# Optimization experiments

Hardware: AMD Instinct MI355X
Metric: run time of the kernel (lower is better)

Reference implementation:

```python
import jax, jax.numpy as jnp
import numpy as np

NUM_HEADS = 16
HEAD_DIM = 64  # hidden_size 1024 / 16 heads


def setup_inputs() -> dict:
    key = jax.random.key(0)
    ks = jax.random.split(key, 9)
    B, T, H = 8, 4096, 1024
    s = 1.0 / np.sqrt(H)
    return {
        "hidden_states": jax.random.normal(ks[0], (B, T + 1, H), jnp.float32),
        "cell_state": jax.random.normal(ks[1], (B, H), jnp.float32),
        "Wq": jax.random.normal(ks[2], (H, H), jnp.float32) * s,
        "bq": jax.random.normal(ks[3], (H,), jnp.float32) * 0.02,
        "Wk": jax.random.normal(ks[4], (H, H), jnp.float32) * s,
        "bk": jax.random.normal(ks[5], (H,), jnp.float32) * 0.02,
        "Wv": jax.random.normal(ks[6], (H, H), jnp.float32) * s,
        "bv": jax.random.normal(ks[7], (H,), jnp.float32) * 0.02,
        "attention_mask": jax.random.randint(ks[8], (B, T), 0, 2, jnp.int32),
        "t": T,
    }


def reference(hidden_states, cell_state, Wq, bq, Wk, bk, Wv, bv, attention_mask, t):
    B, _, H = hidden_states.shape
    nh, hd = NUM_HEADS, HEAD_DIM
    # single-query projection: [B, H] -> [B, nh, hd]
    q = (cell_state @ Wq.T + bq).reshape(B, nh, hd)
    # key/value over first t positions: [B, t, H] -> [B, t, nh, hd]
    kv_in = hidden_states[:, :-1]
    k = (kv_in @ Wk.T + bk).reshape(B, t, nh, hd)
    v = (kv_in @ Wv.T + bv).reshape(B, t, nh, hd)
    # GEMV-like scores: [B, nh, t]
    scores = jnp.einsum("bhd,bthd->bht", q, k) / np.sqrt(hd)
    # mask out positions where attention_mask == 0 (intended semantics of
    # inf * eq(mask, 0) in the original, expressed without -inf*0 NaNs)
    mask_add = jnp.where(attention_mask == 0, -jnp.inf, 0.0)[:, None, :]
    probs = jax.nn.softmax(scores + mask_add, axis=-1)
    # dropout is identity in eval mode
    ctx = jnp.einsum("bht,bthd->bhd", probs, v)  # [B, nh, hd]
    return ctx.reshape(B, nh * hd)  # squeeze of [B, 1, H]
```

## Files before the change

kernel.cpp:

```cpp
#include <hip/hip_runtime.h>
#include <math.h>

#define BB 8
#define TT 4096
#define TP1 4097
#define HH 1024
#define NHD 16

__device__ __forceinline__ float dot4(const float4& a, const float4& b) {
  return a.x*b.x + a.y*b.y + a.z*b.z + a.w*b.w;
}

__global__ __launch_bounds__(256) void k_q(const float* __restrict__ cell,
                                           const float* __restrict__ Wq,
                                           const float* __restrict__ bq,
                                           float* __restrict__ qbuf) {
  __shared__ float cs[BB * HH];
  int tid = threadIdx.x;
  #pragma unroll
  for (int m = 0; m < 8; m++) {
    int idx4 = tid + (m << 8);
    ((float4*)cs)[idx4] = ((const float4*)cell)[idx4];
  }
  __syncthreads();
  int jj = tid >> 6, lane = tid & 63;
  int j = blockIdx.x * 4 + jj;
  float acc[BB];
  #pragma unroll
  for (int b = 0; b < BB; b++) acc[b] = 0.f;
  #pragma unroll
  for (int k = 0; k < 4; k++) {
    int i = (k << 8) + (lane << 2);
    float4 w = *(const float4*)&Wq[(size_t)j * HH + i];
    #pragma unroll
    for (int b = 0; b < BB; b++) acc[b] += dot4(w, *(const float4*)&cs[b * HH + i]);
  }
  #pragma unroll
  for (int b = 0; b < BB; b++) {
    acc[b] += __shfl_xor(acc[b], 1);  acc[b] += __shfl_xor(acc[b], 2);
    acc[b] += __shfl_xor(acc[b], 4);  acc[b] += __shfl_xor(acc[b], 8);
    acc[b] += __shfl_xor(acc[b], 16); acc[b] += __shfl_xor(acc[b], 32);
  }
  if (lane == 0) {
    float bqv = bq[j];
    #pragma unroll
    for (int b = 0; b < BB; b++) qbuf[b * HH + j] = 0.125f * (acc[b] + bqv);
  }
}

__global__ __launch_bounds__(256) void k_qwk(const float* __restrict__ qbuf,
                                             const float* __restrict__ Wk,
                                             const float* __restrict__ bk,
                                             float* __restrict__ qWkT,
                                             float* __restrict__ qbk) {
  __shared__ float q_s[BB * 64];
  __shared__ float red[4 * 64 * 9];
  int tid = threadIdx.x;
  int h = blockIdx.x >> 4, ic = blockIdx.x & 15;
  if (tid < 128) {
    int b = tid >> 4, dq = tid & 15;
    ((float4*)q_s)[tid] = ((const float4*)qbuf)[(b << 8) + (h << 4) + dq];
  }
  __syncthreads();
  int dg = tid >> 6, lane = tid & 63;
  int i = (ic << 6) + lane;
  float acc[BB];
  #pragma unroll
  for (int b = 0; b < BB; b++) acc[b] = 0.f;
  #pragma unroll
  for (int dd = 0; dd < 16; dd++) {
    int d = (dg << 4) + dd;
    float wk = Wk[(size_t)((h << 6) + d) * HH + i];
    #pragma unroll
    for (int b = 0; b < BB; b++) acc[b] += q_s[(b << 6) + d] * wk;
  }
  #pragma unroll
  for (int b = 0; b < BB; b++) red[((dg << 6) + lane) * 9 + b] = acc[b];
  __syncthreads();
  #pragma unroll
  for (int r = 0; r < 2; r++) {
    int o = tid + (r << 8);
    int il = o >> 3, b = o & 7;
    float s = 0.f;
    #pragma unroll
    for (int g = 0; g < 4; g++) s += red[((g << 6) + il) * 9 + b];
    qWkT[((size_t)(b << 10) + (ic << 6) + il) * NHD + h] = s;
  }
  if (ic == 0 && tid < 8) {
    float s = 0.f;
    for (int d = 0; d < 64; d++) s += q_s[(tid << 6) + d] * bk[(h << 6) + d];
    qbk[tid * NHD + h] = s;
  }
}

__global__ __launch_bounds__(512) void k_sctx(const float* __restrict__ hid,
                                              const float* __restrict__ qWkT,
                                              const float* __restrict__ qbk,
                                              const int* __restrict__ mask,
                                              float* __restrict__ ctxp,
                                              float* __restrict__ Spart) {
  __shared__ float S[16384];
  __shared__ float E[1280];
  int tid = threadIdx.x;
  int b = blockIdx.x >> 6, g = blockIdx.x & 63;
  int t0 = g << 6;
  int w = __builtin_amdgcn_readfirstlane(tid >> 6);
  int lane = tid & 63;
  const float* src = hid + ((size_t)b * TP1 + t0) * HH;
  int sub = lane >> 5, q31 = lane & 31;

  #define STAGE(cc, buf)                                                            \
    {                                                                               \
      _Pragma("unroll")                                                             \
      for (int j = 0; j < 4; j++) {                                                 \
        int row0 = (w << 3) + (j << 1);                                             \
        int row = row0 + sub;                                                       \
        const float* gp = src + (size_t)row * HH + ((cc) << 7) +                    \
                          ((q31 ^ (row & 7)) << 2);                                 \
        float* dp = &S[((buf) << 13) + row0 * 128];                                 \
        __builtin_amdgcn_global_load_lds(                                           \
            (const __attribute__((address_space(1))) unsigned int*)gp,              \
            (__attribute__((address_space(3))) unsigned int*)dp, 16, 0, 0);         \
      }                                                                             \
    }

  STAGE(0, 0);
  __syncthreads();

  float acc[16];
  #pragma unroll
  for (int h = 0; h < 16; h++) acc[h] = 0.f;
  const float* qb = qWkT + ((size_t)b << 14);

  for (int c = 0; c < 8; c++) {
    if (c < 7) STAGE(c + 1, (c + 1) & 1);
    const float* sb = &S[(c & 1) << 13];
    #pragma unroll
    for (int s = 0; s < 4; s++) {
      int q = (w << 2) + s;
      float4 kvq = *(const float4*)&sb[lane * 128 + ((q ^ (lane & 7)) << 2)];
      const float* qp = qb + (((size_t)(c << 7) + (q << 2)) << 4);
      #pragma unroll
      for (int ii = 0; ii < 4; ii++) {
        float kvv = (ii == 0) ? kvq.x : (ii == 1) ? kvq.y : (ii == 2) ? kvq.z : kvq.w;
        const float* qi = qp + (ii << 4);
        float4 q0 = *(const float4*)(qi);
        float4 q1 = *(const float4*)(qi + 4);
        float4 q2 = *(const float4*)(qi + 8);
        float4 q3 = *(const float4*)(qi + 12);
        acc[0]  += kvv * q0.x;  acc[1]  += kvv * q0.y;
        acc[2]  += kvv * q0.z;  acc[3]  += kvv * q0.w;
        acc[4]  += kvv * q1.x;  acc[5]  += kvv * q1.y;
        acc[6]  += kvv * q1.z;  acc[7]  += kvv * q1.w;
        acc[8]  += kvv * q2.x;  acc[9]  += kvv * q2.y;
        acc[10] += kvv * q2.z;  acc[11] += kvv * q2.w;
        acc[12] += kvv * q3.x;  acc[13] += kvv * q3.y;
        acc[14] += kvv * q3.z;  acc[15] += kvv * q3.w;
      }
    }
    __syncthreads();
  }

  {
    float* rp = S + w * 1088 + lane * 17;
    #pragma unroll
    for (int h = 0; h < 16; h++) rp[h] = acc[h];
  }
  __syncthreads();

  {
    float s1 = 0.f, s2 = 0.f;
    #pragma unroll
    for (int ww = 0; ww < 8; ww++) {
      s1 += S[ww * 1088 + lane * 17 + w];
      s2 += S[ww * 1088 + lane * 17 + w + 8];
    }
    s1 += qbk[b * NHD + w];
    s2 += qbk[b * NHD + w + 8];
    int mk = mask[b * TT + t0 + lane];
    float e1 = mk ? __expf(s1) : 0.f;
    float e2 = mk ? __expf(s2) : 0.f;
    E[lane * 20 + w] = e1;
    E[lane * 20 + w + 8] = e2;
    float sp1 = e1, sp2 = e2;
    #pragma unroll
    for (int m2 = 1; m2 < 64; m2 <<= 1) {
      sp1 += __shfl_xor(sp1, m2);
      sp2 += __shfl_xor(sp2, m2);
    }
    if (lane == 0) {
      Spart[(((size_t)b << 6) + g) * NHD + w] = sp1;
      Spart[(((size_t)b << 6) + g) * NHD + w + 8] = sp2;
    }
  }
  __syncthreads();

  STAGE(0, 0);
  __syncthreads();

  for (int c = 0; c < 8; c++) {
    if (c < 7) STAGE(c + 1, (c + 1) & 1);
    if (w < 4) {
      float4 p0 = make_float4(0.f, 0.f, 0.f, 0.f);
      float4 p1 = make_float4(0.f, 0.f, 0.f, 0.f);
      float4 p2 = make_float4(0.f, 0.f, 0.f, 0.f);
      float4 p3 = make_float4(0.f, 0.f, 0.f, 0.f);
      const float* sb = &S[(c & 1) << 13];
      #pragma unroll 8
      for (int r = 0; r < 32; r++) {
        int row = (sub << 5) + r;
        float4 kvq = *(const float4*)&sb[row * 128 + ((q31 ^ (row & 7)) << 2)];
        float4 ev  = *(const float4*)&E[row * 20 + (w << 2)];
        p0.x += kvq.x * ev.x; p0.y += kvq.y * ev.x; p0.z += kvq.z * ev.x; p0.w += kvq.w * ev.x;
        p1.x += kvq.x * ev.y; p1.y += kvq.y * ev.y; p1.z += kvq.z * ev.y; p1.w += kvq.w * ev.y;
        p2.x += kvq.x * ev.z; p2.y += kvq.y * ev.z; p2.z += kvq.z * ev.z; p2.w += kvq.w * ev.z;
        p3.x += kvq.x * ev.w; p3.y += kvq.y * ev.w; p3.z += kvq.z * ev.w; p3.w += kvq.w * ev.w;
      }
      p0.x += __shfl_xor(p0.x, 32); p0.y += __shfl_xor(p0.y, 32);
      p0.z += __shfl_xor(p0.z, 32); p0.w += __shfl_xor(p0.w, 32);
      p1.x += __shfl_xor(p1.x, 32); p1.y += __shfl_xor(p1.y, 32);
      p1.z += __shfl_xor(p1.z, 32); p1.w += __shfl_xor(p1.w, 32);
      p2.x += __shfl_xor(p2.x, 32); p2.y += __shfl_xor(p2.y, 32);
      p2.z += __shfl_xor(p2.z, 32); p2.w += __shfl_xor(p2.w, 32);
      p3.x += __shfl_xor(p3.x, 32); p3.y += __shfl_xor(p3.y, 32);
      p3.z += __shfl_xor(p3.z, 32); p3.w += __shfl_xor(p3.w, 32);
      if (sub == 0) {
        float* cp = ctxp + ((((size_t)(b << 6) + g) * NHD + (w << 2)) << 10) +
                    (c << 7) + (q31 << 2);
        *(float4*)(cp)        = p0;
        *(float4*)(cp + 1024) = p1;
        *(float4*)(cp + 2048) = p2;
        *(float4*)(cp + 3072) = p3;
      }
    }
    __syncthreads();
  }
  #undef STAGE
}

__global__ void k_sinv(const float* __restrict__ Spart, float* __restrict__ Sinv) {
  int tid = threadIdx.x;
  int b = tid >> 4, h = tid & 15;
  float s = 0.f;
  #pragma unroll 8
  for (int c = 0; c < 64; c++) s += Spart[(size_t)((b << 6) + c) * NHD + h];
  Sinv[tid] = 1.f / s;
}

__global__ __launch_bounds__(256) void k_reduce(const float* __restrict__ ctxp,
                                                float* __restrict__ ctxin) {
  int tid = threadIdx.x;
  int b = blockIdx.x >> 4, h = blockIdx.x & 15;
  const float4* cp4 = (const float4*)ctxp;
  float4 s = make_float4(0.f, 0.f, 0.f, 0.f);
  #pragma unroll 8
  for (int g = 0; g < 64; g++) {
    float4 v = cp4[((((size_t)b * 64 + g) * 16 + h) << 8) + tid];
    s.x += v.x; s.y += v.y; s.z += v.z; s.w += v.w;
  }
  ((float4*)ctxin)[(((size_t)(b << 4) + h) << 8) + tid] = s;
}

__global__ __launch_bounds__(256) void k_out(const float* __restrict__ Wv,
                                             const float* __restrict__ bv,
                                             const float* __restrict__ ctxin,
                                             const float* __restrict__ Sinv,
                                             float* __restrict__ out) {
  __shared__ float cs[BB * HH];
  int tid = threadIdx.x;
  int h = blockIdx.x >> 4;
  int j0 = blockIdx.x * 4;
  #pragma unroll
  for (int m = 0; m < 8; m++) {
    int idx4 = tid + (m << 8);
    int b = idx4 >> 8, i4 = idx4 & 255;
    ((float4*)cs)[idx4] = ((const float4*)ctxin)[(((b << 4) + h) << 8) + i4];
  }
  __syncthreads();
  int jj = tid >> 6, lane = tid & 63;
  int j = j0 + jj;
  float acc[BB];
  #pragma unroll
  for (int b = 0; b < BB; b++) acc[b] = 0.f;
  #pragma unroll
  for (int k = 0; k < 4; k++) {
    int i = (k << 8) + (lane << 2);
    float4 w = *(const float4*)&Wv[(size_t)j * HH + i];
    #pragma unroll
    for (int b = 0; b < BB; b++) acc[b] += dot4(w, *(const float4*)&cs[b * HH + i]);
  }
  #pragma unroll
  for (int b = 0; b < BB; b++) {
    acc[b] += __shfl_xor(acc[b], 1);  acc[b] += __shfl_xor(acc[b], 2);
    acc[b] += __shfl_xor(acc[b], 4);  acc[b] += __shfl_xor(acc[b], 8);
    acc[b] += __shfl_xor(acc[b], 16); acc[b] += __shfl_xor(acc[b], 32);
  }
  if (lane == 0) {
    float bvj = bv[j];
    #pragma unroll
    for (int b = 0; b < BB; b++)
      out[b * HH + j] = Sinv[b * NHD + h] * acc[b] + bvj;
  }
}

extern "C" void kernel_launch(void* const* d_in, const int* in_sizes, int n_in,
                              void* d_out, int out_size, void* d_ws, size_t ws_size,
                              hipStream_t stream) {
  const float* hid  = (const float*)d_in[0];
  const float* cell = (const float*)d_in[1];
  const float* Wq   = (const float*)d_in[2];
  const float* bq   = (const float*)d_in[3];
  const float* Wk   = (const float*)d_in[4];
  const float* bk   = (const float*)d_in[5];
  const float* Wv   = (const float*)d_in[6];
  const float* bv   = (const float*)d_in[7];
  const int*  mask  = (const int*)d_in[8];
  float* out = (float*)d_out;

  float* ws = (float*)d_ws;
  float* qbuf    = ws;
  float* qWkT    = ws + 8192;
  float* qbk     = ws + 139264;
  float* Spart   = ws + 139392;
  float* Sinv    = ws + 147584;
  float* ctxin   = ws + 147712;
  float* ctxp    = ws + 278784;

  hipLaunchKernelGGL(k_q,      dim3(256), dim3(256), 0, stream, cell, Wq, bq, qbuf);
  hipLaunchKernelGGL(k_qwk,    dim3(256), dim3(256), 0, stream, qbuf, Wk, bk, qWkT, qbk);
  hipLaunchKernelGGL(k_sctx,   dim3(512), dim3(512), 0, stream, hid, qWkT, qbk, mask, ctxp, Spart);
  hipLaunchKernelGGL(k_sinv,   dim3(1),   dim3(128), 0, stream, Spart, Sinv);
  hipLaunchKernelGGL(k_reduce, dim3(128), dim3(256), 0, stream, ctxp, ctxin);
  hipLaunchKernelGGL(k_out,    dim3(256), dim3(256), 0, stream, Wv, bv, ctxin, Sinv, out);
}
```

Baseline: 266.0 us.

## Halve k_sctx LDS staging chunks and fold softmax-sum kernel into k_out

The score/context kernel now stages 64-column chunks instead of 128 (16 chunks instead of 8) and reuses the staging buffer for the exp values, cutting shared memory from about 69KB to about 37KB so more blocks can be resident per CU. The cross-wave score reduction is reworked to fit the smaller buffer, and the PV loop uses 16-lane groups with an extra shuffle stage. The single-block k_sinv launch is removed; k_out sums the partial softmax denominators itself. In exchange there are twice as many barriers and stage loops, and every k_out block repeats the denominator reduction.

```diff
diff --git a/kernel.cpp b/kernel.cpp
--- a/kernel.cpp
+++ b/kernel.cpp
@@ -99,25 +99,25 @@
                                               const int* __restrict__ mask,
                                               float* __restrict__ ctxp,
                                               float* __restrict__ Spart) {
-  __shared__ float S[16384];
-  __shared__ float E[1280];
+  __shared__ float S[9472];
   int tid = threadIdx.x;
   int b = blockIdx.x >> 6, g = blockIdx.x & 63;
   int t0 = g << 6;
   int w = __builtin_amdgcn_readfirstlane(tid >> 6);
   int lane = tid & 63;
   const float* src = hid + ((size_t)b * TP1 + t0) * HH;
-  int sub = lane >> 5, q31 = lane & 31;
+  int rsub = lane >> 4, q15 = lane & 15;
+  #define E_OFF 8192
 
   #define STAGE(cc, buf)                                                            \
     {                                                                               \
       _Pragma("unroll")                                                             \
-      for (int j = 0; j < 4; j++) {                                                 \
-        int row0 = (w << 3) + (j << 1);                                             \
-        int row = row0 + sub;                                                       \
-        const float* gp = src + (size_t)row * HH + ((cc) << 7) +                    \
-                          ((q31 ^ (row & 7)) << 2);                                 \
-        float* dp = &S[((buf) << 13) + row0 * 128];                                 \
+      for (int j = 0; j < 2; j++) {                                                 \
+        int row0 = (w << 3) + (j << 2);                                             \
+        int row = row0 + rsub;                                                      \
+        const float* gp = src + (size_t)row * HH + ((cc) << 6) +                    \
+                          ((q15 ^ (row & 7)) << 2);                                 \
+        float* dp = &S[((buf) << 12) + (row0 << 6)];                                \
         __builtin_amdgcn_global_load_lds(                                           \
             (const __attribute__((address_space(1))) unsigned int*)gp,              \
             (__attribute__((address_space(3))) unsigned int*)dp, 16, 0, 0);         \
@@ -132,14 +132,14 @@
   for (int h = 0; h < 16; h++) acc[h] = 0.f;
   const float* qb = qWkT + ((size_t)b << 14);
 
-  for (int c = 0; c < 8; c++) {
-    if (c < 7) STAGE(c + 1, (c + 1) & 1);
-    const float* sb = &S[(c & 1) << 13];
-    #pragma unroll
-    for (int s = 0; s < 4; s++) {
-      int q = (w << 2) + s;
-      float4 kvq = *(const float4*)&sb[lane * 128 + ((q ^ (lane & 7)) << 2)];
-      const float* qp = qb + (((size_t)(c << 7) + (q << 2)) << 4);
+  for (int c = 0; c < 16; c++) {
+    if (c < 15) STAGE(c + 1, (c + 1) & 1);
+    const float* sb = &S[(c & 1) << 12];
+    #pragma unroll
+    for (int s = 0; s < 2; s++) {
+      int q = (w << 1) + s;
+      float4 kvq = *(const float4*)&sb[(lane << 6) + ((q ^ (lane & 7)) << 2)];
+      const float* qp = qb + (((size_t)(c << 6) + (q << 2)) << 4);
       #pragma unroll
       for (int ii = 0; ii < 4; ii++) {
         float kvv = (ii == 0) ? kvq.x : (ii == 1) ? kvq.y : (ii == 2) ? kvq.z : kvq.w;
@@ -161,27 +161,33 @@
     __syncthreads();
   }
 
-  {
+  if (w >= 4) {
+    float* rp = S + (w - 4) * 1088 + lane * 17;
+    #pragma unroll
+    for (int h = 0; h < 16; h++) rp[h] = acc[h];
+  }
+  __syncthreads();
+  if (w < 4) {
     float* rp = S + w * 1088 + lane * 17;
     #pragma unroll
-    for (int h = 0; h < 16; h++) rp[h] = acc[h];
+    for (int h = 0; h < 16; h++) rp[h] += acc[h];
   }
   __syncthreads();
 
   {
     float s1 = 0.f, s2 = 0.f;
     #pragma unroll
-    for (int ww = 0; ww < 8; ww++) {
-      s1 += S[ww * 1088 + lane * 17 + w];
-      s2 += S[ww * 1088 + lane * 17 + w + 8];
+    for (int ss = 0; ss < 4; ss++) {
+      s1 += S[ss * 1088 + lane * 17 + w];
+      s2 += S[ss * 1088 + lane * 17 + w + 8];
     }
     s1 += qbk[b * NHD + w];
     s2 += qbk[b * NHD + w + 8];
     int mk = mask[b * TT + t0 + lane];
     float e1 = mk ? __expf(s1) : 0.f;
     float e2 = mk ? __expf(s2) : 0.f;
-    E[lane * 20 + w] = e1;
-    E[lane * 20 + w + 8] = e2;
+    S[E_OFF + lane * 20 + w] = e1;
+    S[E_OFF + lane * 20 + w + 8] = e2;
     float sp1 = e1, sp2 = e2;
     #pragma unroll
     for (int m2 = 1; m2 < 64; m2 <<= 1) {
@@ -198,24 +204,32 @@
   STAGE(0, 0);
   __syncthreads();
 
-  for (int c = 0; c < 8; c++) {
-    if (c < 7) STAGE(c + 1, (c + 1) & 1);
+  for (int c = 0; c < 16; c++) {
+    if (c < 15) STAGE(c + 1, (c + 1) & 1);
     if (w < 4) {
       float4 p0 = make_float4(0.f, 0.f, 0.f, 0.f);
       float4 p1 = make_float4(0.f, 0.f, 0.f, 0.f);
       float4 p2 = make_float4(0.f, 0.f, 0.f, 0.f);
       float4 p3 = make_float4(0.f, 0.f, 0.f, 0.f);
-      const float* sb = &S[(c & 1) << 13];
+      const float* sb = &S[(c & 1) << 12];
       #pragma unroll 8
-      for (int r = 0; r < 32; r++) {
-        int row = (sub << 5) + r;
-        float4 kvq = *(const float4*)&sb[row * 128 + ((q31 ^ (row & 7)) << 2)];
-        float4 ev  = *(const float4*)&E[row * 20 + (w << 2)];
+      for (int rr = 0; rr < 16; rr++) {
+        int row = (rsub << 4) + rr;
+        float4 kvq = *(const float4*)&sb[(row << 6) + ((q15 ^ (row & 7)) << 2)];
+        float4 ev  = *(const float4*)&S[E_OFF + row * 20 + (w << 2)];
         p0.x += kvq.x * ev.x; p0.y += kvq.y * ev.x; p0.z += kvq.z * ev.x; p0.w += kvq.w * ev.x;
         p1.x += kvq.x * ev.y; p1.y += kvq.y * ev.y; p1.z += kvq.z * ev.y; p1.w += kvq.w * ev.y;
         p2.x += kvq.x * ev.z; p2.y += kvq.y * ev.z; p2.z += kvq.z * ev.z; p2.w += kvq.w * ev.z;
         p3.x += kvq.x * ev.w; p3.y += kvq.y * ev.w; p3.z += kvq.z * ev.w; p3.w += kvq.w * ev.w;
       }
+      p0.x += __shfl_xor(p0.x, 16); p0.y += __shfl_xor(p0.y, 16);
+      p0.z += __shfl_xor(p0.z, 16); p0.w += __shfl_xor(p0.w, 16);
+      p1.x += __shfl_xor(p1.x, 16); p1.y += __shfl_xor(p1.y, 16);
+      p1.z += __shfl_xor(p1.z, 16); p1.w += __shfl_xor(p1.w, 16);
+      p2.x += __shfl_xor(p2.x, 16); p2.y += __shfl_xor(p2.y, 16);
+      p2.z += __shfl_xor(p2.z, 16); p2.w += __shfl_xor(p2.w, 16);
+      p3.x += __shfl_xor(p3.x, 16); p3.y += __shfl_xor(p3.y, 16);
+      p3.z += __shfl_xor(p3.z, 16); p3.w += __shfl_xor(p3.w, 16);
       p0.x += __shfl_xor(p0.x, 32); p0.y += __shfl_xor(p0.y, 32);
       p0.z += __shfl_xor(p0.z, 32); p0.w += __shfl_xor(p0.w, 32);
       p1.x += __shfl_xor(p1.x, 32); p1.y += __shfl_xor(p1.y, 32);
@@ -224,9 +238,9 @@
       p2.z += __shfl_xor(p2.z, 32); p2.w += __shfl_xor(p2.w, 32);
       p3.x += __shfl_xor(p3.x, 32); p3.y += __shfl_xor(p3.y, 32);
       p3.z += __shfl_xor(p3.z, 32); p3.w += __shfl_xor(p3.w, 32);
-      if (sub == 0) {
+      if (lane < 16) {
         float* cp = ctxp + ((((size_t)(b << 6) + g) * NHD + (w << 2)) << 10) +
-                    (c << 7) + (q31 << 2);
+                    (c << 6) + (lane << 2);
         *(float4*)(cp)        = p0;
         *(float4*)(cp + 1024) = p1;
         *(float4*)(cp + 2048) = p2;
@@ -236,15 +250,7 @@
     __syncthreads();
   }
   #undef STAGE
-}
-
-__global__ void k_sinv(const float* __restrict__ Spart, float* __restrict__ Sinv) {
-  int tid = threadIdx.x;
-  int b = tid >> 4, h = tid & 15;
-  float s = 0.f;
-  #pragma unroll 8
-  for (int c = 0; c < 64; c++) s += Spart[(size_t)((b << 6) + c) * NHD + h];
-  Sinv[tid] = 1.f / s;
+  #undef E_OFF
 }
 
 __global__ __launch_bounds__(256) void k_reduce(const float* __restrict__ ctxp,
@@ -264,9 +270,10 @@
 __global__ __launch_bounds__(256) void k_out(const float* __restrict__ Wv,
                                              const float* __restrict__ bv,
                                              const float* __restrict__ ctxin,
-                                             const float* __restrict__ Sinv,
+                                             const float* __restrict__ Spart,
                                              float* __restrict__ out) {
   __shared__ float cs[BB * HH];
+  __shared__ float sp2[64];
   int tid = threadIdx.x;
   int h = blockIdx.x >> 4;
   int j0 = blockIdx.x * 4;
@@ -276,6 +283,14 @@
     int b = idx4 >> 8, i4 = idx4 & 255;
     ((float4*)cs)[idx4] = ((const float4*)ctxin)[(((b << 4) + h) << 8) + i4];
   }
+  if (tid < 64) {
+    int bb = tid >> 3, gg = tid & 7;
+    float s = 0.f;
+    #pragma unroll
+    for (int k = 0; k < 8; k++)
+      s += Spart[(size_t)((bb << 6) + (gg << 3) + k) * NHD + h];
+    sp2[tid] = s;
+  }
   __syncthreads();
   int jj = tid >> 6, lane = tid & 63;
   int j = j0 + jj;
@@ -298,8 +313,12 @@
   if (lane == 0) {
     float bvj = bv[j];
     #pragma unroll
-    for (int b = 0; b < BB; b++)
-      out[b * HH + j] = Sinv[b * NHD + h] * acc[b] + bvj;
+    for (int b = 0; b < BB; b++) {
+      float sv = 0.f;
+      #pragma unroll
+      for (int k = 0; k < 8; k++) sv += sp2[(b << 3) + k];
+      out[b * HH + j] = acc[b] / sv + bvj;
+    }
   }
 }
 
@@ -322,14 +341,12 @@
   float* qWkT    = ws + 8192;
   float* qbk     = ws + 139264;
   float* Spart   = ws + 139392;
-  float* Sinv    = ws + 147584;
-  float* ctxin   = ws + 147712;
-  float* ctxp    = ws + 278784;
+  float* ctxin   = ws + 147584;
+  float* ctxp    = ws + 278656;
 
   hipLaunchKernelGGL(k_q,      dim3(256), dim3(256), 0, stream, cell, Wq, bq, qbuf);
   hipLaunchKernelGGL(k_qwk,    dim3(256), dim3(256), 0, stream, qbuf, Wk, bk, qWkT, qbk);
   hipLaunchKernelGGL(k_sctx,   dim3(512), dim3(512), 0, stream, hid, qWkT, qbk, mask, ctxp, Spart);
-  hipLaunchKernelGGL(k_sinv,   dim3(1),   dim3(128), 0, stream, Spart, Sinv);
   hipLaunchKernelGGL(k_reduce, dim3(128), dim3(256), 0, stream, ctxp, ctxin);
-  hipLaunchKernelGGL(k_out,    dim3(256), dim3(256), 0, stream, Wv, bv, ctxin, Sinv, out);
-}
+  hipLaunchKernelGGL(k_out,    dim3(256), dim3(256), 0, stream, Wv, bv, ctxin, Spart, out);
+}
```

After: 271.7 us. +2.1%, slower.
